# Kernel tuning notes

Hardware: AMD Instinct MI355X
Metric: run time of the kernel (lower is better)

## Reference

```python
import jax, jax.numpy as jnp
import numpy as np

NH, HD, MBS = 32, 64, 16   # num_heads, head_dim, mini_batch_size
BASE_LR = 1.0
ROPE_BASE = 10000.0
EPS = 1e-6


def _rotate_half(x):
    x1, x2 = jnp.split(x, 2, axis=-1)
    return jnp.concatenate((-x2, x1), axis=-1)


def _permute_qk(x):
    B, H, L, D = x.shape
    return x.reshape(B, H, L, D // 2, 2).swapaxes(-1, -2).reshape(B, H, L, D)


def _undo_permute_qk(x):
    B, H, L, D = x.shape
    return x.reshape(B, H, L, 2, D // 2).swapaxes(-1, -2).reshape(B, H, L, D)


def _ln_fwd(x, gamma, beta):
    mu = x.mean(-1, keepdims=True)
    var = x.var(-1, keepdims=True)
    return gamma * ((x - mu) / jnp.sqrt(var + EPS)) + beta


def _ln_fused_l2_bwd(x, target, gamma, beta):
    # grad of 0.5*||LN(x) - target||^2 wrt x, fused
    D = x.shape[-1]
    mu = x.mean(-1, keepdims=True)
    std = jnp.sqrt(x.var(-1, keepdims=True) + EPS)
    x_hat = (x - mu) / std
    y = gamma * x_hat + beta
    g = (y - target) * gamma
    return (D * g - g.sum(-1, keepdims=True) - x_hat * (g * x_hat).sum(-1, keepdims=True)) / (D * std)


def setup_inputs() -> dict:
    key = jax.random.key(0)
    ks = jax.random.split(key, 8)
    B, L, C, OUT = 4, 2048, 2048, 768
    s = 0.02
    return {
        "hidden_states": jax.random.normal(ks[0], (B, L, C), jnp.float32),
        "position_ids": jnp.broadcast_to(jnp.arange(L, dtype=jnp.int32)[None], (B, L)),
        "Wq": jax.random.normal(ks[1], (C, C), jnp.float32) * s,
        "Wk": jax.random.normal(ks[2], (C, C), jnp.float32) * s,
        "Wv": jax.random.normal(ks[3], (C, C), jnp.float32) * s,
        "Wo": jax.random.normal(ks[4], (C, OUT), jnp.float32) * s,
        "W1": jax.random.normal(ks[5], (NH, HD, HD), jnp.float32) * s,
        "b1": jnp.zeros((NH, 1, HD), jnp.float32),
        "ttt_lr_weight": jax.random.normal(ks[6], (NH, 1, C), jnp.float32) * s,
        "ttt_lr_bias": jnp.zeros((NH, 1), jnp.float32),
        "learnable_token_idx": jnp.zeros((MBS,), jnp.float32),
        "ttt_norm_weight": jnp.ones((NH, HD), jnp.float32),
        "ttt_norm_bias": jnp.zeros((NH, HD), jnp.float32),
        "post_norm_weight": jnp.ones((C,), jnp.float32),
        "post_norm_bias": jnp.zeros((C,), jnp.float32),
    }


def reference(hidden_states, position_ids, Wq, Wk, Wv, Wo, W1, b1,
              ttt_lr_weight, ttt_lr_bias, learnable_token_idx,
              ttt_norm_weight, ttt_norm_bias, post_norm_weight, post_norm_bias):
    B, L, C = hidden_states.shape
    NM = L // MBS
    # QKV projections -> [B, NH, L, HD]
    XQ = (hidden_states @ Wq).reshape(B, L, NH, HD).transpose(0, 2, 1, 3)
    XK = (hidden_states @ Wk).reshape(B, L, NH, HD).transpose(0, 2, 1, 3)
    XV = (hidden_states @ Wv).reshape(B, L, NH, HD).transpose(0, 2, 1, 3)
    # RoPE on positions modulo the mini-batch size
    pos = (position_ids % MBS).astype(jnp.float32)  # [B, L]
    inv_freq = 1.0 / (ROPE_BASE ** (jnp.arange(0, HD, 2, dtype=jnp.float32) / HD))
    freqs = pos[..., None] * inv_freq               # [B, L, HD/2]
    emb = jnp.concatenate((freqs, freqs), axis=-1)  # [B, L, HD]
    cos = jnp.cos(emb)[:, None]                     # [B, 1, L, HD]
    sin = jnp.sin(emb)[:, None]
    XQ, XK = _permute_qk(XQ), _permute_qk(XK)
    XQ = XQ * cos + _rotate_half(XQ) * sin
    XK = XK * cos + _rotate_half(XK) * sin
    XQ, XK = _undo_permute_qk(XQ), _undo_permute_qk(XK)
    # reshape into mini-batches: [B, NH, NM, K, HD]
    X = hidden_states.reshape(B, NM, MBS, C)
    XQ = XQ.reshape(B, NH, NM, MBS, HD)
    XK = XK.reshape(B, NH, NM, MBS, HD)
    XV = XV.reshape(B, NH, NM, MBS, HD)
    # eta: per-token learnable LR gate
    ttt_lr = jax.nn.sigmoid(
        jnp.einsum('bnkc,hdc->bhnkd', X, ttt_lr_weight)
        + ttt_lr_bias.reshape(1, NH, 1, 1, 1))              # [B,NH,NM,K,1]
    ttt_lr_eta = BASE_LR * ttt_lr.transpose(0, 1, 2, 4, 3) / HD  # [B,NH,NM,1,K]
    token_idx = jnp.clip(1.0 / jnp.arange(1, MBS + 1, dtype=jnp.float32)
                         + learnable_token_idx, 0.0, None)
    token_eta = token_idx.reshape(1, 1, 1, MBS, 1)
    eta = token_eta * ttt_lr_eta                            # [B,NH,NM,K,K]
    # TTT-Linear dual-form mini-batch scan
    ln_w = ttt_norm_weight.reshape(1, NH, 1, HD)
    ln_b = ttt_norm_bias.reshape(1, NH, 1, HD)
    W1_0 = jnp.broadcast_to(W1[None], (B, NH, HD, HD))
    b1_0 = jnp.broadcast_to(b1[None], (B, NH, 1, HD))
    tril = jnp.tril(jnp.ones((MBS, MBS), hidden_states.dtype))

    def step(carry, xs):
        W1_s, b1_s = carry
        xq, xk, xv, eta_m = xs                 # [B,NH,K,HD], eta_m [B,NH,K,K]
        Z1 = xk @ W1_s + b1_s
        target = xv - xk
        grad = _ln_fused_l2_bwd(Z1, target, ln_w, ln_b)
        Attn = tril * (xq @ xk.swapaxes(-1, -2))
        b1_bar = b1_s - (tril * eta_m) @ grad
        Z1_bar = xq @ W1_s - (eta_m * Attn) @ grad + b1_bar
        last_eta = eta_m[:, :, -1, :, None]    # [B,NH,K,1]
        W1_new = W1_s - (last_eta * xk).swapaxes(-1, -2) @ grad
        b1_new = b1_s - jnp.sum(last_eta * grad, axis=-2, keepdims=True)
        out = xq + _ln_fwd(Z1_bar, ln_w, ln_b)
        return (W1_new, b1_new), out

    xs = (XQ.transpose(2, 0, 1, 3, 4), XK.transpose(2, 0, 1, 3, 4),
          XV.transpose(2, 0, 1, 3, 4), eta.transpose(2, 0, 1, 3, 4))
    _, outs = jax.lax.scan(step, (W1_0, b1_0), xs)   # [NM,B,NH,K,HD]
    out = outs.transpose(1, 2, 0, 3, 4).reshape(B, NH, L, HD)
    out = out.transpose(0, 2, 1, 3).reshape(B, L, C)
    # post LayerNorm (eps 1e-6) and output projection
    mu = out.mean(-1, keepdims=True)
    var = out.var(-1, keepdims=True)
    out = (out - mu) / jnp.sqrt(var + EPS) * post_norm_weight + post_norm_bias
    return out @ Wo
```

## Files before the change

kernel.cpp:

```cpp
#include <hip/hip_runtime.h>
#include <cstddef>
#include <cstdint>

#define B_DIM   4
#define L_SEQ   2048
#define C_DIM   2048
#define OUT_DIM 768
#define NHEADS  32
#define HDIM    64
#define MBS_    16
#define NMINI   128
#define EPS_    1e-6f

typedef _Float16 half8 __attribute__((ext_vector_type(8)));
typedef _Float16 half4 __attribute__((ext_vector_type(4)));
typedef float floatx4 __attribute__((ext_vector_type(4)));

__device__ __forceinline__ void glds16(const void* g, void* l) {
    __builtin_amdgcn_global_load_lds(
        (const __attribute__((address_space(1))) uint32_t*)g,
        (__attribute__((address_space(3))) uint32_t*)l, 16, 0, 0);
}

__device__ __forceinline__ void split8(const float4 a, const float4 b,
                                       half8& hi, half8& lo) {
    const float x[8] = {a.x, a.y, a.z, a.w, b.x, b.y, b.z, b.w};
#pragma unroll
    for (int e = 0; e < 8; e++) {
        const _Float16 h = (_Float16)x[e];
        hi[e] = h;
        lo[e] = (_Float16)(x[e] - (float)h);
    }
}

__device__ __forceinline__ void split4(const float4 a, half4& hi, half4& lo) {
    const float x[4] = {a.x, a.y, a.z, a.w};
#pragma unroll
    for (int e = 0; e < 4; e++) {
        const _Float16 h = (_Float16)x[e];
        hi[e] = h;
        lo[e] = (_Float16)(x[e] - (float)h);
    }
}

__global__ __launch_bounds__(256)
void gemm_af32(const float* __restrict__ A,
               const _Float16* __restrict__ Bhi, const _Float16* __restrict__ Blo,
               float* __restrict__ Cout, int mode, int doRope)
{
    __shared__ __align__(16) float    sA[4096];
    __shared__ __align__(16) _Float16 sBhi[4096];
    __shared__ __align__(16) _Float16 sBlo[4096];
    const int tid = threadIdx.x;
    const int m0 = blockIdx.y * 128, n0 = blockIdx.x * 128;
    const int K = 2048;

    size_t gA[4]; float* lA[4];
#pragma unroll
    for (int I = 0; I < 4; I++) {
        const int c = I * 256 + tid;
        const int row = c >> 3, seg = (c & 7) ^ (row & 7);
        gA[I] = (size_t)(m0 + row) * K + seg * 4;
        lA[I] = &sA[c * 4];
    }
    size_t gB[2]; _Float16 *lBh[2], *lBl[2];
#pragma unroll
    for (int I = 0; I < 2; I++) {
        const int c = I * 256 + tid;
        const int row = c >> 2, seg = (c & 3) ^ ((row >> 1) & 3);
        gB[I] = (size_t)(n0 + row) * K + seg * 8;
        lBh[I] = &sBhi[c * 8];
        lBl[I] = &sBlo[c * 8];
    }

    const int lane = tid & 63, quad = lane >> 4, lc = lane & 15;
    const int wv = tid >> 6, wm = wv & 1, wn = wv >> 1;
    int offA0[4], offA1[4], offB[4];
#pragma unroll
    for (int i = 0; i < 4; i++) {
        const int rA = wm * 64 + i * 16 + lc;
        offA0[i] = (rA * 8 + ((2 * quad)     ^ (rA & 7))) * 4;
        offA1[i] = (rA * 8 + ((2 * quad + 1) ^ (rA & 7))) * 4;
    }
#pragma unroll
    for (int j = 0; j < 4; j++) {
        const int rB = wn * 64 + j * 16 + lc;
        offB[j] = (rB * 4 + (quad ^ ((rB >> 1) & 3))) * 8;
    }

    floatx4 acc[4][4];
#pragma unroll
    for (int i = 0; i < 4; i++)
#pragma unroll
        for (int j = 0; j < 4; j++) acc[i][j] = (floatx4)0.0f;

    for (int k0 = 0; k0 < K; k0 += 32) {
        __syncthreads();
#pragma unroll
        for (int I = 0; I < 4; I++) glds16(A + gA[I] + k0, lA[I]);
#pragma unroll
        for (int I = 0; I < 2; I++) {
            glds16(Bhi + gB[I] + k0, lBh[I]);
            glds16(Blo + gB[I] + k0, lBl[I]);
        }
        __syncthreads();

        half8 ah[4], al[4], bh[4], bl[4];
#pragma unroll
        for (int i = 0; i < 4; i++) {
            const float4 va = *(const float4*)&sA[offA0[i]];
            const float4 vb = *(const float4*)&sA[offA1[i]];
            split8(va, vb, ah[i], al[i]);
        }
#pragma unroll
        for (int j = 0; j < 4; j++) {
            bh[j] = *(const half8*)&sBhi[offB[j]];
            bl[j] = *(const half8*)&sBlo[offB[j]];
        }
#pragma unroll
        for (int i = 0; i < 4; i++)
#pragma unroll
            for (int j = 0; j < 4; j++) {
                acc[i][j] = __builtin_amdgcn_mfma_f32_16x16x32_f16(ah[i], bh[j], acc[i][j], 0, 0, 0);
                acc[i][j] = __builtin_amdgcn_mfma_f32_16x16x32_f16(ah[i], bl[j], acc[i][j], 0, 0, 0);
                acc[i][j] = __builtin_amdgcn_mfma_f32_16x16x32_f16(al[i], bh[j], acc[i][j], 0, 0, 0);
            }
    }

    float cs[4][4], sn[4][4];
    if (doRope) {
#pragma unroll
        for (int j = 0; j < 4; j++) {
            const int ii = ((j * 16 + lc) & 63) >> 1;
            const float invf = expf(-(float)ii * 0.28782313662425574f);
#pragma unroll
            for (int r = 0; r < 4; r++) {
                const float ang = (float)(quad * 4 + r) * invf;
                sincosf(ang, &sn[j][r], &cs[j][r]);
            }
        }
    }
    const int oddcol = lc & 1;
#pragma unroll
    for (int i = 0; i < 4; i++) {
#pragma unroll
        for (int j = 0; j < 4; j++) {
            floatx4 v = acc[i][j];
            if (doRope) {
#pragma unroll
                for (int r = 0; r < 4; r++) {
                    const float partner = __shfl_xor(v[r], 1);
                    v[r] = v[r] * cs[j][r] + partner * (oddcol ? sn[j][r] : -sn[j][r]);
                }
            }
            const int n = n0 + wn * 64 + j * 16 + lc;
            if (mode == 0) {
                const int h = (n >> 6) & 31, d = n & 63;
#pragma unroll
                for (int r = 0; r < 4; r++) {
                    const int m = m0 + wm * 64 + i * 16 + quad * 4 + r;
                    const int b = m >> 11, li = m & 2047;
                    Cout[((size_t)(b * 32 + h) * 2048 + li) * 64 + d] = v[r];
                }
            } else {
#pragma unroll
                for (int r = 0; r < 4; r++) {
                    const int m = m0 + wm * 64 + i * 16 + quad * 4 + r;
                    Cout[(size_t)m * OUT_DIM + n] = v[r];
                }
            }
        }
    }
}

__global__ __launch_bounds__(256)
void wtrans_kernel(const float* __restrict__ W, _Float16* __restrict__ BThi,
                   _Float16* __restrict__ BTlo, int Nw)
{
    __shared__ float tile[32][33];
    const int t = threadIdx.x, tx = t & 31, ty = t >> 5;
    const int n0 = blockIdx.x * 32, k0 = blockIdx.y * 32;
    const int K = 2048;
#pragma unroll
    for (int r = 0; r < 4; r++)
        tile[ty + r * 8][tx] = W[(size_t)(k0 + ty + r * 8) * Nw + n0 + tx];
    __syncthreads();
#pragma unroll
    for (int r = 0; r < 4; r++) {
        const float val = tile[tx][ty + r * 8];
        const _Float16 hh = (_Float16)val;
        const size_t o = (size_t)(n0 + ty + r * 8) * K + k0 + tx;
        BThi[o] = hh;
        BTlo[o] = (_Float16)(val - (float)hh);
    }
}

__global__ __launch_bounds__(256)
void lr_kernel(const float* __restrict__ hidden, const float* __restrict__ wlr,
               const float* __restrict__ lr_bias, float* __restrict__ lrs)
{
    __shared__ float sRow[2048];
    __shared__ float sPart[32][9];
    const int m = blockIdx.x;
    const int t = threadIdx.x;
    const float* row = hidden + (size_t)m * C_DIM;
#pragma unroll
    for (int j = 0; j < 8; j++) sRow[t + j * 256] = row[t + j * 256];
    __syncthreads();
    const int h = t >> 3, p = t & 7;
    const float* w = wlr + (size_t)h * C_DIM;
    float s = 0.0f;
#pragma unroll 8
    for (int k = 0; k < 64; k++) {
        const int c = k * 32 + p * 4;
        const float4 a = *(const float4*)(sRow + c);
        const float4 b = *(const float4*)(w + c);
        s += a.x * b.x + a.y * b.y + a.z * b.z + a.w * b.w;
    }
    sPart[h][p] = s;
    __syncthreads();
    if (t < 32) {
        float v = 0.0f;
#pragma unroll
        for (int p2 = 0; p2 < 8; p2++) v += sPart[t][p2];
        v += lr_bias[t];
        const float sig = 1.0f / (1.0f + expf(-v));
        lrs[((size_t)(m >> 11) * NHEADS + t) * L_SEQ + (m & 2047)] = sig;
    }
}

__global__ __launch_bounds__(256, 1)
void scan_mfma(const float* __restrict__ XQ, const float* __restrict__ XK,
               float* __restrict__ XVo, const float* __restrict__ LRS,
               const float* __restrict__ W1i, const float* __restrict__ b1i,
               const float* __restrict__ lt, const float* __restrict__ lnw,
               const float* __restrict__ lnb)
{
    __shared__ __align__(16) _Float16 sXqH[2][1024], sXqL[2][1024];
    __shared__ __align__(16) _Float16 sXkH[1024], sXkL[1024];
    __shared__ __align__(16) float    sXv[16 * 68];
    __shared__ __align__(16) _Float16 sW1H[4096], sW1L[4096];
    __shared__ __align__(16) _Float16 sGtH[2560], sGtL[2560];
    __shared__ __align__(16) _Float16 sKtH[2560], sKtL[2560];
    __shared__ __align__(16) _Float16 sCfH[640],  sCfL[640];
    __shared__ __align__(16) float sRedA[128], sRedB[128], sRedC[128];
    __shared__ float sEta[32], sB1[64];

    const int bh = blockIdx.x, h = bh & 31;
    const int t = threadIdx.x;
    const int lane = t & 63, q = lane >> 4, lc = lane & 15;
    const int w = t >> 6;
    const int col = w * 16 + lc;
    const int iRow = t >> 4;
    const int m = t & 15;

    if (t < 64) sB1[t] = b1i[h * 64 + t];
    if (t < 32) sEta[t] = 0.0f;
    for (int idx = t; idx < 64 * 24; idx += 256) {
        const int nn = idx / 24, j = 16 + idx % 24;
        sGtH[nn * 40 + j] = (_Float16)0.0f; sGtL[nn * 40 + j] = (_Float16)0.0f;
        sKtH[nn * 40 + j] = (_Float16)0.0f; sKtL[nn * 40 + j] = (_Float16)0.0f;
    }
    for (int idx = t; idx < 16 * 24; idx += 256) {
        const int ii = idx / 24, j = 16 + idx % 24;
        sCfH[ii * 40 + j] = (_Float16)0.0f; sCfL[ii * 40 + j] = (_Float16)0.0f;
    }

    float w1s[4][4];
#pragma unroll
    for (int t4 = 0; t4 < 4; t4++)
#pragma unroll
        for (int r = 0; r < 4; r++) {
            const float v = W1i[h * 4096 + (16 * t4 + lc) * 64 + (16 * w + 4 * q + r)];
            w1s[t4][r] = v;
            const int nn = 16 * w + 4 * q + r, k = 16 * t4 + lc;
            const int off = nn * 64 + ((((k >> 3) ^ (nn & 7)) << 3) | (k & 7));
            const _Float16 hh = (_Float16)v;
            sW1H[off] = hh; sW1L[off] = (_Float16)(v - (float)hh);
        }

    const float gamC = lnw[h * 64 + col], betC = lnb[h * 64 + col];
    float tokR[4];
#pragma unroll
    for (int r = 0; r < 4; r++)
        tokR[r] = fmaxf(1.0f / (float)(4 * q + r + 1) + lt[4 * q + r], 0.0f);
    const float tok15 = fmaxf(1.0f / 16.0f + lt[15], 0.0f);

    __syncthreads();

    const size_t base = (size_t)bh * L_SEQ * HDIM;
    const float* xq_g = XQ + base;
    const float* xk_g = XK + base;
    float* xv_g = XVo + base;
    const float* lr_g = LRS + (size_t)bh * L_SEQ;

    float4 cq = *(const float4*)(xq_g + t * 4);
    float4 ck = *(const float4*)(xk_g + t * 4);
    float4 cv = *(const float4*)(xv_g + t * 4);
    float clr = lr_g[m];

    const int rw = 16 * w + lc;

    for (int n = 0; n < NMINI; n++) {
        const int buf = n & 1;
        {
            half4 hq, lq, hk, lk;
            split4(cq, hq, lq);
            split4(ck, hk, lk);
            const int off = iRow * 64 + ((((m >> 1) ^ (iRow & 7)) << 3) | ((m & 1) << 2));
            *(half4*)&sXqH[buf][off] = hq;
            *(half4*)&sXqL[buf][off] = lq;
            *(half4*)&sXkH[off] = hk;
            *(half4*)&sXkL[off] = lk;
            *(float4*)&sXv[iRow * 68 + m * 4] = cv;
        }
        if (t < 16) sEta[t] = clr * (1.0f / 64.0f);
        const int np = (n + 1) & (NMINI - 1);
        const float4 nq = *(const float4*)(xq_g + np * 1024 + t * 4);
        const float4 nk = *(const float4*)(xk_g + np * 1024 + t * 4);
        const float4 nv = *(const float4*)(xv_g + np * 1024 + t * 4);
        const float nlr = lr_g[np * 16 + m];
        __syncthreads();

        {
            const float le = tok15 * sEta[iRow];
            const float kvv[4] = {ck.x, ck.y, ck.z, ck.w};
#pragma unroll
            for (int i2 = 0; i2 < 4; i2++) {
                const float v = kvv[i2] * le;
                const _Float16 hh = (_Float16)v;
                const int o2 = (4 * m + i2) * 40 + iRow;
                sKtH[o2] = hh; sKtL[o2] = (_Float16)(v - (float)hh);
            }
        }
        const float b1c = sB1[col];
        const float4 ev0 = *(const float4*)&sEta[8 * q];
        const float4 ev1 = *(const float4*)&sEta[8 * q + 4];

        half8 qh[2], ql[2], kh[2], kl[2], wh[2], wl[2];
#pragma unroll
        for (int f = 0; f < 2; f++) {
            const int cx = ((4 * f + q) ^ (lc & 7)) << 3;
            qh[f] = *(const half8*)&sXqH[buf][lc * 64 + cx];
            ql[f] = *(const half8*)&sXqL[buf][lc * 64 + cx];
            kh[f] = *(const half8*)&sXkH[lc * 64 + cx];
            kl[f] = *(const half8*)&sXkL[lc * 64 + cx];
            const int cw = ((4 * f + q) ^ (rw & 7)) << 3;
            wh[f] = *(const half8*)&sW1H[rw * 64 + cw];
            wl[f] = *(const half8*)&sW1L[rw * 64 + cw];
        }

        floatx4 z1a = (floatx4)0.0f, zba = (floatx4)0.0f, at = (floatx4)0.0f;
#pragma unroll
        for (int f = 0; f < 2; f++) {
            z1a = __builtin_amdgcn_mfma_f32_16x16x32_f16(kh[f], wh[f], z1a, 0, 0, 0);
            z1a = __builtin_amdgcn_mfma_f32_16x16x32_f16(kh[f], wl[f], z1a, 0, 0, 0);
            z1a = __builtin_amdgcn_mfma_f32_16x16x32_f16(kl[f], wh[f], z1a, 0, 0, 0);
            zba = __builtin_amdgcn_mfma_f32_16x16x32_f16(qh[f], wh[f], zba, 0, 0, 0);
            zba = __builtin_amdgcn_mfma_f32_16x16x32_f16(qh[f], wl[f], zba, 0, 0, 0);
            zba = __builtin_amdgcn_mfma_f32_16x16x32_f16(ql[f], wh[f], zba, 0, 0, 0);
        }
        if (w == 0) {
            const float etaLC = sEta[lc];
#pragma unroll
            for (int f = 0; f < 2; f++) {
                at = __builtin_amdgcn_mfma_f32_16x16x32_f16(qh[f], kh[f], at, 0, 0, 0);
                at = __builtin_amdgcn_mfma_f32_16x16x32_f16(qh[f], kl[f], at, 0, 0, 0);
                at = __builtin_amdgcn_mfma_f32_16x16x32_f16(ql[f], kh[f], at, 0, 0, 0);
            }
#pragma unroll
            for (int r = 0; r < 4; r++) {
                const int i = 4 * q + r;
                const float cf = (lc <= i) ? -tokR[r] * etaLC * (at[r] + 1.0f) : 0.0f;
                const _Float16 hh = (_Float16)cf;
                sCfH[i * 40 + lc] = hh;
                sCfL[i * 40 + lc] = (_Float16)(cf - (float)hh);
            }
        }

        float z[4], s1[4], s2[4];
#pragma unroll
        for (int r = 0; r < 4; r++) { z[r] = z1a[r] + b1c; s1[r] = z[r]; s2[r] = z[r] * z[r]; }
#pragma unroll
        for (int o = 1; o < 16; o <<= 1)
#pragma unroll
            for (int r = 0; r < 4; r++) { s1[r] += __shfl_xor(s1[r], o); s2[r] += __shfl_xor(s2[r], o); }
        if (lc == 0)
#pragma unroll
            for (int r = 0; r < 4; r++) {
                sRedA[(4 * q + r) * 8 + w] = s1[r];
                sRedA[(4 * q + r) * 8 + 4 + w] = s2[r];
            }
        __syncthreads();

        const half8 cfh = *(const half8*)&sCfH[lc * 40 + 8 * q];
        const half8 cfl = *(const half8*)&sCfL[lc * 40 + 8 * q];
        half8 kth[4], ktl[4];
#pragma unroll
        for (int t4 = 0; t4 < 4; t4++) {
            kth[t4] = *(const half8*)&sKtH[(16 * t4 + lc) * 40 + 8 * q];
            ktl[t4] = *(const half8*)&sKtL[(16 * t4 + lc) * 40 + 8 * q];
        }
        float muR[4], rsR[4];
#pragma unroll
        for (int r = 0; r < 4; r++) {
            const int row = 4 * q + r;
            const float4 a = *(const float4*)&sRedA[row * 8];
            const float4 b = *(const float4*)&sRedA[row * 8 + 4];
            const float mu = (a.x + a.y + a.z + a.w) * (1.0f / 64.0f);
            const float ex2 = (b.x + b.y + b.z + b.w) * (1.0f / 64.0f);
            muR[r] = mu;
            rsR[r] = rsqrtf(ex2 - mu * mu + EPS_);
        }

        float gg[4], xh[4];
#pragma unroll
        for (int r = 0; r < 4; r++) {
            const int row = 4 * q + r;
            xh[r] = (z[r] - muR[r]) * rsR[r];
            const int ok = row * 64 + ((((col >> 3) ^ (row & 7)) << 3) | (col & 7));
            const float xkv = (float)sXkH[ok] + (float)sXkL[ok];
            const float tgt = sXv[row * 68 + col] - xkv;
            gg[r] = (gamC * xh[r] + betC - tgt) * gamC;
            s1[r] = gg[r]; s2[r] = gg[r] * xh[r];
        }
#pragma unroll
        for (int o = 1; o < 16; o <<= 1)
#pragma unroll
            for (int r = 0; r < 4; r++) { s1[r] += __shfl_xor(s1[r], o); s2[r] += __shfl_xor(s2[r], o); }
        if (lc == 0)
#pragma unroll
            for (int r = 0; r < 4; r++) {
                sRedB[(4 * q + r) * 8 + w] = s1[r];
                sRedB[(4 * q + r) * 8 + 4 + w] = s2[r];
            }
        __syncthreads();

#pragma unroll
        for (int r = 0; r < 4; r++) {
            const int row = 4 * q + r;
            const float4 a = *(const float4*)&sRedB[row * 8];
            const float4 b = *(const float4*)&sRedB[row * 8 + 4];
            const float G1 = a.x + a.y + a.z + a.w;
            const float G2 = b.x + b.y + b.z + b.w;
            const float gr = (64.0f * gg[r] - G1 - xh[r] * G2) * rsR[r] * (1.0f / 64.0f);
            const _Float16 hh = (_Float16)gr;
            sGtH[col * 40 + row] = hh;
            sGtL[col * 40 + row] = (_Float16)(gr - (float)hh);
        }
        const half8 gth = *(const half8*)&sGtH[rw * 40 + 8 * q];
        const half8 gtl = *(const half8*)&sGtL[rw * 40 + 8 * q];

        zba = __builtin_amdgcn_mfma_f32_16x16x32_f16(cfh, gth, zba, 0, 0, 0);
        zba = __builtin_amdgcn_mfma_f32_16x16x32_f16(cfh, gtl, zba, 0, 0, 0);
        zba = __builtin_amdgcn_mfma_f32_16x16x32_f16(cfl, gth, zba, 0, 0, 0);
#pragma unroll
        for (int t4 = 0; t4 < 4; t4++) {
            floatx4 up = (floatx4)0.0f;
            up = __builtin_amdgcn_mfma_f32_16x16x32_f16(gth, kth[t4], up, 0, 0, 0);
            up = __builtin_amdgcn_mfma_f32_16x16x32_f16(gth, ktl[t4], up, 0, 0, 0);
            up = __builtin_amdgcn_mfma_f32_16x16x32_f16(gtl, kth[t4], up, 0, 0, 0);
#pragma unroll
            for (int r = 0; r < 4; r++) w1s[t4][r] -= up[r];
        }

        float z2[4];
#pragma unroll
        for (int r = 0; r < 4; r++) { z2[r] = zba[r] + b1c; s1[r] = z2[r]; s2[r] = z2[r] * z2[r]; }
#pragma unroll
        for (int o = 1; o < 16; o <<= 1)
#pragma unroll
            for (int r = 0; r < 4; r++) { s1[r] += __shfl_xor(s1[r], o); s2[r] += __shfl_xor(s2[r], o); }
        if (lc == 0)
#pragma unroll
            for (int r = 0; r < 4; r++) {
                sRedC[(4 * q + r) * 8 + w] = s1[r];
                sRedC[(4 * q + r) * 8 + 4 + w] = s2[r];
            }
        __syncthreads();

#pragma unroll
        for (int r = 0; r < 4; r++) {
            const int row = 4 * q + r;
            const float4 a = *(const float4*)&sRedC[row * 8];
            const float4 b = *(const float4*)&sRedC[row * 8 + 4];
            const float mu = (a.x + a.y + a.z + a.w) * (1.0f / 64.0f);
            const float ex2 = (b.x + b.y + b.z + b.w) * (1.0f / 64.0f);
            const float rs = rsqrtf(ex2 - mu * mu + EPS_);
            const int oq = row * 64 + ((((col >> 3) ^ (row & 7)) << 3) | (col & 7));
            const float xqv = (float)sXqH[buf][oq] + (float)sXqL[buf][oq];
            xv_g[n * 1024 + row * 64 + col] = xqv + gamC * ((z2[r] - mu) * rs) + betC;
        }

        {
            const float evv[8] = {ev0.x, ev0.y, ev0.z, ev0.w, ev1.x, ev1.y, ev1.z, ev1.w};
            float p = 0.0f;
#pragma unroll
            for (int jj = 0; jj < 8; jj++)
                p += ((float)gth[jj] + (float)gtl[jj]) * evv[jj];
            p += __shfl_xor(p, 16);
            if (q == 0) sB1[col] -= tok15 * p;
        }

#pragma unroll
        for (int t4 = 0; t4 < 4; t4++)
#pragma unroll
            for (int r = 0; r < 4; r++) {
                const int nn = 16 * w + 4 * q + r, k = 16 * t4 + lc;
                const int off = nn * 64 + ((((k >> 3) ^ (nn & 7)) << 3) | (k & 7));
                const float v = w1s[t4][r];
                const _Float16 hh = (_Float16)v;
                sW1H[off] = hh; sW1L[off] = (_Float16)(v - (float)hh);
            }
        cq = nq; ck = nk; cv = nv; clr = nlr;
    }
}

__global__ __launch_bounds__(256)
void postln_kernel(const float* __restrict__ Ob, const float* __restrict__ pnw,
                   const float* __restrict__ pnb, float* __restrict__ XN)
{
    const int m = blockIdx.x;
    const int b = m >> 11, l = m & 2047;
    const int t = threadIdx.x;
    float v[8];
    float s1 = 0.0f, s2 = 0.0f;
    const float* bas = Ob + (size_t)b * NHEADS * L_SEQ * HDIM + (size_t)l * HDIM;
#pragma unroll
    for (int j = 0; j < 8; j++) {
        const int c = t + j * 256;
        const int hh = c >> 6, d = c & 63;
        const float x = bas[(size_t)hh * (L_SEQ * HDIM) + d];
        v[j] = x; s1 += x; s2 += x * x;
    }
#pragma unroll
    for (int o = 1; o < 64; o <<= 1) { s1 += __shfl_xor(s1, o); s2 += __shfl_xor(s2, o); }
    __shared__ float r1[4], r2[4];
    const int w = t >> 6;
    if ((t & 63) == 0) { r1[w] = s1; r2[w] = s2; }
    __syncthreads();
    s1 = r1[0] + r1[1] + r1[2] + r1[3];
    s2 = r2[0] + r2[1] + r2[2] + r2[3];
    const float mu = s1 * (1.0f / 2048.0f);
    const float var = s2 * (1.0f / 2048.0f) - mu * mu;
    const float rstd = rsqrtf(var + EPS_);
    float* o = XN + (size_t)m * C_DIM;
#pragma unroll
    for (int j = 0; j < 8; j++) {
        const int c = t + j * 256;
        o[c] = (v[j] - mu) * rstd * pnw[c] + pnb[c];
    }
}

extern "C" void kernel_launch(void* const* d_in, const int* in_sizes, int n_in,
                              void* d_out, int out_size, void* d_ws, size_t ws_size,
                              hipStream_t stream)
{
    (void)in_sizes; (void)n_in; (void)out_size;
    const float* hidden  = (const float*)d_in[0];
    const float* Wq      = (const float*)d_in[2];
    const float* Wk      = (const float*)d_in[3];
    const float* Wv      = (const float*)d_in[4];
    const float* Wo      = (const float*)d_in[5];
    const float* W1      = (const float*)d_in[6];
    const float* b1      = (const float*)d_in[7];
    const float* wlr     = (const float*)d_in[8];
    const float* lr_bias = (const float*)d_in[9];
    const float* lt      = (const float*)d_in[10];
    const float* lnw     = (const float*)d_in[11];
    const float* lnb     = (const float*)d_in[12];
    const float* pnw     = (const float*)d_in[13];
    const float* pnb     = (const float*)d_in[14];

    const size_t TEN = (size_t)B_DIM * NHEADS * L_SEQ * HDIM;
    float* XQ  = (float*)d_ws;
    float* XK  = XQ + TEN;
    float* XVo = XK + TEN;
    float* LRS = XVo + TEN;
    const dim3 blk(256);

    _Float16* BThi = (_Float16*)d_out;
    _Float16* BTlo = BThi + (size_t)C_DIM * C_DIM;

    lr_kernel<<<dim3(B_DIM * L_SEQ), blk, 0, stream>>>(hidden, wlr, lr_bias, LRS);

    const float* Wmats[3] = {Wq, Wk, Wv};
    float* outs[3] = {XQ, XK, XVo};
    for (int p = 0; p < 3; p++) {
        wtrans_kernel<<<dim3(64, 64), blk, 0, stream>>>(Wmats[p], BThi, BTlo, C_DIM);
        gemm_af32<<<dim3(16, 64), blk, 0, stream>>>(hidden, BThi, BTlo,
                                                    outs[p], 0, (p < 2) ? 1 : 0);
    }
    scan_mfma<<<dim3(B_DIM * NHEADS), blk, 0, stream>>>(XQ, XK, XVo, LRS,
                                                        W1, b1, lt, lnw, lnb);
    float* XN = XQ;
    _Float16* WThi = (_Float16*)XK;
    _Float16* WTlo = WThi + (size_t)OUT_DIM * C_DIM;
    postln_kernel<<<dim3(B_DIM * L_SEQ), blk, 0, stream>>>(XVo, pnw, pnb, XN);
    wtrans_kernel<<<dim3(24, 64), blk, 0, stream>>>(Wo, WThi, WTlo, OUT_DIM);
    gemm_af32<<<dim3(6, 64), blk, 0, stream>>>(XN, WThi, WTlo,
                                               (float*)d_out, 1, 0);
}
```

Before: 1.510 ms.

## Cut scan barriers via single-pass LN-backward stats, DPP reductions, packed hi/lo operands

Restructures the per-minibatch scan loop. The LayerNorm-backward statistics (G1, G2) are rewritten algebraically in terms of sums of z, z^2 and target-dependent terms, so one reduction round replaces two. The 16-lane shuffle reductions become DPP adds, and the hi/lo fp16 pairs are packed into interleaved words so each error-compensated MFMA product takes two instructions instead of three. Barriers drop from four to three per step, and the output write moves after the final barrier. The expanded moment formulas may lose floating-point accuracy, and the packed hi/lo trick is an approximation that drops the lo*lo term in a different way than before.

```diff
diff --git a/kernel.cpp b/kernel.cpp
--- a/kernel.cpp
+++ b/kernel.cpp
@@ -41,6 +41,39 @@
         hi[e] = h;
         lo[e] = (_Float16)(x[e] - (float)h);
     }
+}
+
+__device__ __forceinline__ uint32_t pack_hl(float v) {
+    const _Float16 h = (_Float16)v;
+    const _Float16 l = (_Float16)(v - (float)h);
+    union { _Float16 f[2]; uint32_t u; } p;
+    p.f[0] = h; p.f[1] = l;
+    return p.u;
+}
+
+__device__ __forceinline__ half8 pairswap(half8 v) {
+    union { half8 h; uint32_t u[4]; } a, b;
+    a.h = v;
+#pragma unroll
+    for (int e = 0; e < 4; e++) b.u[e] = (a.u[e] >> 16) | (a.u[e] << 16);
+    return b.h;
+}
+
+template<int CTRL>
+__device__ __forceinline__ float dpp_add(float v) {
+    const int x = __builtin_amdgcn_update_dpp(0, __float_as_int(v), CTRL, 0xF, 0xF, false);
+    return v + __int_as_float(x);
+}
+__device__ __forceinline__ float red16(float v) {
+    v = dpp_add<0xB1>(v);
+    v = dpp_add<0x4E>(v);
+    v = dpp_add<0x124>(v);
+    v = dpp_add<0x128>(v);
+    return v;
+}
+
+__device__ __forceinline__ void bar_lgkm() {
+    asm volatile("s_waitcnt lgkmcnt(0)\n\ts_barrier" ::: "memory");
 }
 
 __global__ __launch_bounds__(256)
@@ -236,15 +269,17 @@
                const float* __restrict__ lt, const float* __restrict__ lnw,
                const float* __restrict__ lnb)
 {
-    __shared__ __align__(16) _Float16 sXqH[2][1024], sXqL[2][1024];
+    __shared__ __align__(16) _Float16 sXqH[1024], sXqL[1024];
     __shared__ __align__(16) _Float16 sXkH[1024], sXkL[1024];
-    __shared__ __align__(16) float    sXv[16 * 68];
+    __shared__ __align__(16) float    sTgt[16 * 68];
+    __shared__ __align__(16) float    sXq32[2][16 * 68];
     __shared__ __align__(16) _Float16 sW1H[4096], sW1L[4096];
-    __shared__ __align__(16) _Float16 sGtH[2560], sGtL[2560];
-    __shared__ __align__(16) _Float16 sKtH[2560], sKtL[2560];
-    __shared__ __align__(16) _Float16 sCfH[640],  sCfL[640];
-    __shared__ __align__(16) float sRedA[128], sRedB[128], sRedC[128];
-    __shared__ float sEta[32], sB1[64];
+    __shared__ __align__(16) uint32_t sKT[64 * 20];
+    __shared__ __align__(16) uint32_t sCf[16 * 20];
+    __shared__ __align__(16) float sRedA[16 * 36];
+    __shared__ __align__(16) float sRedC[16 * 12];
+    __shared__ __align__(16) float sEta[16];
+    __shared__ float sB1[64];
 
     const int bh = blockIdx.x, h = bh & 31;
     const int t = threadIdx.x;
@@ -255,16 +290,6 @@
     const int m = t & 15;
 
     if (t < 64) sB1[t] = b1i[h * 64 + t];
-    if (t < 32) sEta[t] = 0.0f;
-    for (int idx = t; idx < 64 * 24; idx += 256) {
-        const int nn = idx / 24, j = 16 + idx % 24;
-        sGtH[nn * 40 + j] = (_Float16)0.0f; sGtL[nn * 40 + j] = (_Float16)0.0f;
-        sKtH[nn * 40 + j] = (_Float16)0.0f; sKtL[nn * 40 + j] = (_Float16)0.0f;
-    }
-    for (int idx = t; idx < 16 * 24; idx += 256) {
-        const int ii = idx / 24, j = 16 + idx % 24;
-        sCfH[ii * 40 + j] = (_Float16)0.0f; sCfL[ii * 40 + j] = (_Float16)0.0f;
-    }
 
     float w1s[4][4];
 #pragma unroll
@@ -280,6 +305,13 @@
         }
 
     const float gamC = lnw[h * 64 + col], betC = lnb[h * 64 + col];
+    const float g2c = gamC * gamC;
+    float sumG2 = 0.0f;
+#pragma unroll
+    for (int d0 = 0; d0 < 16; d0++) {
+        const float4 gv = *(const float4*)(lnw + h * 64 + d0 * 4);
+        sumG2 += gv.x * gv.x + gv.y * gv.y + gv.z * gv.z + gv.w * gv.w;
+    }
     float tokR[4];
 #pragma unroll
     for (int r = 0; r < 4; r++)
@@ -300,6 +332,9 @@
     float clr = lr_g[m];
 
     const int rw = 16 * w + lc;
+    const int stOff = iRow * 64 + ((((m >> 1) ^ (iRow & 7)) << 3) | ((m & 1) << 2));
+    const int gkm = (m ^ (m >> 2)) & 3;
+    const int ktWb = 4 * (w ^ gkm) + q;
 
     for (int n = 0; n < NMINI; n++) {
         const int buf = n & 1;
@@ -307,12 +342,18 @@
             half4 hq, lq, hk, lk;
             split4(cq, hq, lq);
             split4(ck, hk, lk);
-            const int off = iRow * 64 + ((((m >> 1) ^ (iRow & 7)) << 3) | ((m & 1) << 2));
-            *(half4*)&sXqH[buf][off] = hq;
-            *(half4*)&sXqL[buf][off] = lq;
-            *(half4*)&sXkH[off] = hk;
-            *(half4*)&sXkL[off] = lk;
-            *(float4*)&sXv[iRow * 68 + m * 4] = cv;
+            *(half4*)&sXqH[stOff] = hq;
+            *(half4*)&sXqL[stOff] = lq;
+            *(half4*)&sXkH[stOff] = hk;
+            *(half4*)&sXkL[stOff] = lk;
+            const float4 tg = make_float4(cv.x - ck.x, cv.y - ck.y,
+                                          cv.z - ck.z, cv.w - ck.w);
+            *(float4*)&sTgt[iRow * 68 + m * 4] = tg;
+            *(float4*)&sXq32[buf][iRow * 68 + m * 4] = cq;
+            const float kvv[4] = {ck.x, ck.y, ck.z, ck.w};
+#pragma unroll
+            for (int i2 = 0; i2 < 4; i2++)
+                sKT[(4 * m + i2) * 20 + ktWb] = pack_hl(kvv[i2]);
         }
         if (t < 16) sEta[t] = clr * (1.0f / 64.0f);
         const int np = (n + 1) & (NMINI - 1);
@@ -320,29 +361,18 @@
         const float4 nk = *(const float4*)(xk_g + np * 1024 + t * 4);
         const float4 nv = *(const float4*)(xv_g + np * 1024 + t * 4);
         const float nlr = lr_g[np * 16 + m];
-        __syncthreads();
-
-        {
-            const float le = tok15 * sEta[iRow];
-            const float kvv[4] = {ck.x, ck.y, ck.z, ck.w};
-#pragma unroll
-            for (int i2 = 0; i2 < 4; i2++) {
-                const float v = kvv[i2] * le;
-                const _Float16 hh = (_Float16)v;
-                const int o2 = (4 * m + i2) * 40 + iRow;
-                sKtH[o2] = hh; sKtL[o2] = (_Float16)(v - (float)hh);
-            }
-        }
+        bar_lgkm();
+
         const float b1c = sB1[col];
-        const float4 ev0 = *(const float4*)&sEta[8 * q];
-        const float4 ev1 = *(const float4*)&sEta[8 * q + 4];
+        const float4 ev = *(const float4*)&sEta[4 * q];
+        const float evv[4] = {ev.x, ev.y, ev.z, ev.w};
 
         half8 qh[2], ql[2], kh[2], kl[2], wh[2], wl[2];
 #pragma unroll
         for (int f = 0; f < 2; f++) {
             const int cx = ((4 * f + q) ^ (lc & 7)) << 3;
-            qh[f] = *(const half8*)&sXqH[buf][lc * 64 + cx];
-            ql[f] = *(const half8*)&sXqL[buf][lc * 64 + cx];
+            qh[f] = *(const half8*)&sXqH[lc * 64 + cx];
+            ql[f] = *(const half8*)&sXqL[lc * 64 + cx];
             kh[f] = *(const half8*)&sXkH[lc * 64 + cx];
             kl[f] = *(const half8*)&sXkL[lc * 64 + cx];
             const int cw = ((4 * f + q) ^ (rw & 7)) << 3;
@@ -371,137 +401,122 @@
 #pragma unroll
             for (int r = 0; r < 4; r++) {
                 const int i = 4 * q + r;
-                const float cf = (lc <= i) ? -tokR[r] * etaLC * (at[r] + 1.0f) : 0.0f;
-                const _Float16 hh = (_Float16)cf;
-                sCfH[i * 40 + lc] = hh;
-                sCfL[i * 40 + lc] = (_Float16)(cf - (float)hh);
-            }
-        }
-
-        float z[4], s1[4], s2[4];
-#pragma unroll
-        for (int r = 0; r < 4; r++) { z[r] = z1a[r] + b1c; s1[r] = z[r]; s2[r] = z[r] * z[r]; }
-#pragma unroll
-        for (int o = 1; o < 16; o <<= 1)
-#pragma unroll
-            for (int r = 0; r < 4; r++) { s1[r] += __shfl_xor(s1[r], o); s2[r] += __shfl_xor(s2[r], o); }
-        if (lc == 0)
-#pragma unroll
-            for (int r = 0; r < 4; r++) {
-                sRedA[(4 * q + r) * 8 + w] = s1[r];
-                sRedA[(4 * q + r) * 8 + 4 + w] = s2[r];
-            }
-        __syncthreads();
-
-        const half8 cfh = *(const half8*)&sCfH[lc * 40 + 8 * q];
-        const half8 cfl = *(const half8*)&sCfL[lc * 40 + 8 * q];
-        half8 kth[4], ktl[4];
-#pragma unroll
-        for (int t4 = 0; t4 < 4; t4++) {
-            kth[t4] = *(const half8*)&sKtH[(16 * t4 + lc) * 40 + 8 * q];
-            ktl[t4] = *(const half8*)&sKtL[(16 * t4 + lc) * 40 + 8 * q];
-        }
-        float muR[4], rsR[4];
+                const float cfv = (lc <= i) ? -tokR[r] * etaLC * (at[r] + 1.0f) : 0.0f;
+                sCf[i * 20 + 4 * ((lc >> 2) ^ q) + (lc & 3)] = pack_hl(cfv);
+            }
+        }
+
+        float z[4], cE[4];
+        float sz[4], szz[4], sgz[4], sgzz[4], sc[4], scz[4];
 #pragma unroll
         for (int r = 0; r < 4; r++) {
             const int row = 4 * q + r;
-            const float4 a = *(const float4*)&sRedA[row * 8];
-            const float4 b = *(const float4*)&sRedA[row * 8 + 4];
-            const float mu = (a.x + a.y + a.z + a.w) * (1.0f / 64.0f);
-            const float ex2 = (b.x + b.y + b.z + b.w) * (1.0f / 64.0f);
-            muR[r] = mu;
-            rsR[r] = rsqrtf(ex2 - mu * mu + EPS_);
-        }
-
-        float gg[4], xh[4];
+            z[r] = z1a[r] + b1c;
+            const float tgt = sTgt[row * 68 + col];
+            cE[r] = gamC * (betC - tgt);
+            const float zz = z[r] * z[r];
+            sz[r]   = red16(z[r]);
+            szz[r]  = red16(zz);
+            sgz[r]  = red16(g2c * z[r]);
+            sgzz[r] = red16(g2c * zz);
+            sc[r]   = red16(cE[r]);
+            scz[r]  = red16(cE[r] * z[r]);
+        }
+        if (lc == 0) {
+#pragma unroll
+            for (int r = 0; r < 4; r++) {
+                const int rb = (4 * q + r) * 36;
+                sRedA[rb + 0  + w] = sz[r];
+                sRedA[rb + 4  + w] = szz[r];
+                sRedA[rb + 8  + w] = sgz[r];
+                sRedA[rb + 12 + w] = sgzz[r];
+                sRedA[rb + 16 + w] = sc[r];
+                sRedA[rb + 20 + w] = scz[r];
+            }
+        }
+        bar_lgkm();
+
+        half8 ktp[4];
+#pragma unroll
+        for (int t4 = 0; t4 < 4; t4++) {
+            const int gkr = ((lc >> 2) ^ t4) & 3;
+            ktp[t4] = *(const half8*)&sKT[(16 * t4 + lc) * 20 + 4 * (q ^ gkr)];
+        }
+        const half8 cfp = *(const half8*)&sCf[lc * 20 + 4 * (q ^ (lc >> 2))];
+
+        float gr[4];
 #pragma unroll
         for (int r = 0; r < 4; r++) {
-            const int row = 4 * q + r;
-            xh[r] = (z[r] - muR[r]) * rsR[r];
-            const int ok = row * 64 + ((((col >> 3) ^ (row & 7)) << 3) | (col & 7));
-            const float xkv = (float)sXkH[ok] + (float)sXkL[ok];
-            const float tgt = sXv[row * 68 + col] - xkv;
-            gg[r] = (gamC * xh[r] + betC - tgt) * gamC;
-            s1[r] = gg[r]; s2[r] = gg[r] * xh[r];
-        }
-#pragma unroll
-        for (int o = 1; o < 16; o <<= 1)
-#pragma unroll
-            for (int r = 0; r < 4; r++) { s1[r] += __shfl_xor(s1[r], o); s2[r] += __shfl_xor(s2[r], o); }
-        if (lc == 0)
-#pragma unroll
-            for (int r = 0; r < 4; r++) {
-                sRedB[(4 * q + r) * 8 + w] = s1[r];
-                sRedB[(4 * q + r) * 8 + 4 + w] = s2[r];
-            }
-        __syncthreads();
-
+            const int rb = (4 * q + r) * 36;
+            const float4 a0 = *(const float4*)&sRedA[rb + 0];
+            const float4 a1 = *(const float4*)&sRedA[rb + 4];
+            const float4 a2 = *(const float4*)&sRedA[rb + 8];
+            const float4 a3 = *(const float4*)&sRedA[rb + 12];
+            const float4 a4 = *(const float4*)&sRedA[rb + 16];
+            const float4 a5 = *(const float4*)&sRedA[rb + 20];
+            const float Sz   = a0.x + a0.y + a0.z + a0.w;
+            const float Szz  = a1.x + a1.y + a1.z + a1.w;
+            const float Sgz  = a2.x + a2.y + a2.z + a2.w;
+            const float Sgzz = a3.x + a3.y + a3.z + a3.w;
+            const float Sc   = a4.x + a4.y + a4.z + a4.w;
+            const float Scz  = a5.x + a5.y + a5.z + a5.w;
+            const float mu  = Sz * (1.0f / 64.0f);
+            const float ex2 = Szz * (1.0f / 64.0f);
+            const float rs  = rsqrtf(ex2 - mu * mu + EPS_);
+            const float G1 = rs * (Sgz - mu * sumG2) + Sc;
+            const float G2 = rs * rs * (Sgzz - 2.0f * mu * Sgz + mu * mu * sumG2)
+                           + rs * (Scz - mu * Sc);
+            const float xh = (z[r] - mu) * rs;
+            const float g  = g2c * xh + cE[r];
+            gr[r] = (64.0f * g - G1 - xh * G2) * rs * (1.0f / 64.0f);
+        }
+
+        half8 gf, gfl;
 #pragma unroll
         for (int r = 0; r < 4; r++) {
-            const int row = 4 * q + r;
-            const float4 a = *(const float4*)&sRedB[row * 8];
-            const float4 b = *(const float4*)&sRedB[row * 8 + 4];
-            const float G1 = a.x + a.y + a.z + a.w;
-            const float G2 = b.x + b.y + b.z + b.w;
-            const float gr = (64.0f * gg[r] - G1 - xh[r] * G2) * rsR[r] * (1.0f / 64.0f);
-            const _Float16 hh = (_Float16)gr;
-            sGtH[col * 40 + row] = hh;
-            sGtL[col * 40 + row] = (_Float16)(gr - (float)hh);
-        }
-        const half8 gth = *(const half8*)&sGtH[rw * 40 + 8 * q];
-        const half8 gtl = *(const half8*)&sGtL[rw * 40 + 8 * q];
-
-        zba = __builtin_amdgcn_mfma_f32_16x16x32_f16(cfh, gth, zba, 0, 0, 0);
-        zba = __builtin_amdgcn_mfma_f32_16x16x32_f16(cfh, gtl, zba, 0, 0, 0);
-        zba = __builtin_amdgcn_mfma_f32_16x16x32_f16(cfl, gth, zba, 0, 0, 0);
+            const _Float16 h0 = (_Float16)gr[r];
+            gf[2 * r]     = h0;
+            gf[2 * r + 1] = (_Float16)(gr[r] - (float)h0);
+            const float gl = gr[r] * (tok15 * evv[r]);
+            const _Float16 h1 = (_Float16)gl;
+            gfl[2 * r]     = h1;
+            gfl[2 * r + 1] = (_Float16)(gl - (float)h1);
+        }
+        const half8 gfs  = pairswap(gf);
+        const half8 gfls = pairswap(gfl);
+
+        zba = __builtin_amdgcn_mfma_f32_16x16x32_f16(cfp, gf,  zba, 0, 0, 0);
+        zba = __builtin_amdgcn_mfma_f32_16x16x32_f16(cfp, gfs, zba, 0, 0, 0);
 #pragma unroll
         for (int t4 = 0; t4 < 4; t4++) {
             floatx4 up = (floatx4)0.0f;
-            up = __builtin_amdgcn_mfma_f32_16x16x32_f16(gth, kth[t4], up, 0, 0, 0);
-            up = __builtin_amdgcn_mfma_f32_16x16x32_f16(gth, ktl[t4], up, 0, 0, 0);
-            up = __builtin_amdgcn_mfma_f32_16x16x32_f16(gtl, kth[t4], up, 0, 0, 0);
+            up = __builtin_amdgcn_mfma_f32_16x16x32_f16(gfl,  ktp[t4], up, 0, 0, 0);
+            up = __builtin_amdgcn_mfma_f32_16x16x32_f16(gfls, ktp[t4], up, 0, 0, 0);
 #pragma unroll
             for (int r = 0; r < 4; r++) w1s[t4][r] -= up[r];
         }
 
-        float z2[4];
-#pragma unroll
-        for (int r = 0; r < 4; r++) { z2[r] = zba[r] + b1c; s1[r] = z2[r]; s2[r] = z2[r] * z2[r]; }
-#pragma unroll
-        for (int o = 1; o < 16; o <<= 1)
-#pragma unroll
-            for (int r = 0; r < 4; r++) { s1[r] += __shfl_xor(s1[r], o); s2[r] += __shfl_xor(s2[r], o); }
+        float z2[4], p1[4], p2[4];
+#pragma unroll
+        for (int r = 0; r < 4; r++) {
+            z2[r] = zba[r] + b1c;
+            p1[r] = red16(z2[r]);
+            p2[r] = red16(z2[r] * z2[r]);
+        }
         if (lc == 0)
 #pragma unroll
             for (int r = 0; r < 4; r++) {
-                sRedC[(4 * q + r) * 8 + w] = s1[r];
-                sRedC[(4 * q + r) * 8 + 4 + w] = s2[r];
-            }
-        __syncthreads();
-
-#pragma unroll
-        for (int r = 0; r < 4; r++) {
-            const int row = 4 * q + r;
-            const float4 a = *(const float4*)&sRedC[row * 8];
-            const float4 b = *(const float4*)&sRedC[row * 8 + 4];
-            const float mu = (a.x + a.y + a.z + a.w) * (1.0f / 64.0f);
-            const float ex2 = (b.x + b.y + b.z + b.w) * (1.0f / 64.0f);
-            const float rs = rsqrtf(ex2 - mu * mu + EPS_);
-            const int oq = row * 64 + ((((col >> 3) ^ (row & 7)) << 3) | (col & 7));
-            const float xqv = (float)sXqH[buf][oq] + (float)sXqL[buf][oq];
-            xv_g[n * 1024 + row * 64 + col] = xqv + gamC * ((z2[r] - mu) * rs) + betC;
-        }
+                const int rb = (4 * q + r) * 12;
+                sRedC[rb + w]     = p1[r];
+                sRedC[rb + 4 + w] = p2[r];
+            }
 
         {
-            const float evv[8] = {ev0.x, ev0.y, ev0.z, ev0.w, ev1.x, ev1.y, ev1.z, ev1.w};
-            float p = 0.0f;
-#pragma unroll
-            for (int jj = 0; jj < 8; jj++)
-                p += ((float)gth[jj] + (float)gtl[jj]) * evv[jj];
+            float p = gr[0] * evv[0] + gr[1] * evv[1] + gr[2] * evv[2] + gr[3] * evv[3];
             p += __shfl_xor(p, 16);
+            p += __shfl_xor(p, 32);
             if (q == 0) sB1[col] -= tok15 * p;
         }
-
 #pragma unroll
         for (int t4 = 0; t4 < 4; t4++)
 #pragma unroll
@@ -512,6 +527,19 @@
                 const _Float16 hh = (_Float16)v;
                 sW1H[off] = hh; sW1L[off] = (_Float16)(v - (float)hh);
             }
+        bar_lgkm();
+
+#pragma unroll
+        for (int r = 0; r < 4; r++) {
+            const int row = 4 * q + r;
+            const float4 a = *(const float4*)&sRedC[row * 12];
+            const float4 b = *(const float4*)&sRedC[row * 12 + 4];
+            const float mu  = (a.x + a.y + a.z + a.w) * (1.0f / 64.0f);
+            const float ex2 = (b.x + b.y + b.z + b.w) * (1.0f / 64.0f);
+            const float rs  = rsqrtf(ex2 - mu * mu + EPS_);
+            const float xqv = sXq32[buf][row * 68 + col];
+            xv_g[n * 1024 + row * 64 + col] = xqv + gamC * ((z2[r] - mu) * rs) + betC;
+        }
         cq = nq; ck = nk; cv = nv; clr = nlr;
     }
 }
```

Measured after the change: 1.423 ms. 1.06x faster.
